# Kernel tuning notes

Measured on AMD Instinct MI355X. Metric: run time of the kernel, lower is better.

Reference implementation:

```python
import jax, jax.numpy as jnp
import numpy as np

H = 2048
EPS = 1e-5

def _layernorm(x, g, b):
    mu = jnp.mean(x, axis=-1, keepdims=True)
    var = jnp.mean(jnp.square(x - mu), axis=-1, keepdims=True)
    return (x - mu) * jax.lax.rsqrt(var + EPS) * g + b

def setup_inputs() -> dict:
    key = jax.random.key(0)
    ks = jax.random.split(key, 12)
    s = 1.0 / np.sqrt(H)
    inp = {
        "x": jax.random.normal(ks[0], (2, 2048, H), dtype=jnp.float32),
        "ln1_g": jnp.ones((H,), jnp.float32),
        "ln1_b": jnp.zeros((H,), jnp.float32),
        "ln2_g": jnp.ones((H,), jnp.float32),
        "ln2_b": jnp.zeros((H,), jnp.float32),
        "qkv_w": jax.random.uniform(ks[1], (H, 3 * H), jnp.float32, -s, s),
        "qkv_b": jax.random.uniform(ks[2], (3 * H,), jnp.float32, -s, s),
        "out_w": jax.random.uniform(ks[3], (H, H), jnp.float32, -s, s),
        "out_b": jax.random.uniform(ks[4], (H,), jnp.float32, -s, s),
        "mlp_w1": jax.random.uniform(ks[5], (H, 4 * H), jnp.float32, -s, s),
        "mlp_b1": jax.random.uniform(ks[6], (4 * H,), jnp.float32, -s, s),
        "mlp_w2": jax.random.uniform(ks[7], (4 * H, H), jnp.float32, -1.0 / np.sqrt(4 * H), 1.0 / np.sqrt(4 * H)),
        "mlp_b2": jax.random.uniform(ks[8], (H,), jnp.float32, -1.0 / np.sqrt(4 * H), 1.0 / np.sqrt(4 * H)),
    }
    return inp

def reference(x, ln1_g, ln1_b, ln2_g, ln2_b, qkv_w, qkv_b, out_w, out_b, mlp_w1, mlp_b1, mlp_w2, mlp_b2):
    residual = x
    h = _layernorm(x, ln1_g, ln1_b)
    qkv = h @ qkv_w + qkv_b                      # [B,S,3H]
    q, k, v = jnp.split(qkv, 3, axis=-1)         # each [B,S,H] (single-head attention)
    scores = jnp.einsum('bsh,bth->bst', q, k) / jnp.sqrt(jnp.float32(H))
    attn = jax.nn.softmax(scores, axis=-1)
    attn_out = jnp.einsum('bst,bth->bsh', attn, v)
    attn_out = attn_out @ out_w + out_b
    x = residual + attn_out                      # dropout is identity in eval
    residual = x
    h = _layernorm(x, ln2_g, ln2_b)
    h = jax.nn.gelu(h @ mlp_w1 + mlp_b1, approximate=False)
    h = h @ mlp_w2 + mlp_b2
    return residual + h
```

## Files before the change

### kernel.cpp

```cpp
#include <hip/hip_runtime.h>
#include <hip/hip_bf16.h>
#include <math.h>

typedef __bf16 bf16_t;
typedef __bf16 bf16x8 __attribute__((ext_vector_type(8)));
typedef __bf16 bf16x4 __attribute__((ext_vector_type(4)));
typedef float  f32x4  __attribute__((ext_vector_type(4)));

enum { EPI_BF16_BIAS = 0, EPI_F32_SCALE = 1, EPI_BF16 = 2, EPI_F32_BIAS_RES = 3, EPI_BF16_BIAS_GELU = 4 };

__device__ __forceinline__ float gelu_exact(float v) {
  return 0.5f * v * (1.0f + erff(v * 0.7071067811865476f));
}

__device__ __forceinline__ void gld_lds16(const bf16_t* g, bf16_t* l) {
  __builtin_amdgcn_global_load_lds(
      (const __attribute__((address_space(1))) uint32_t*)(uintptr_t)g,
      (__attribute__((address_space(3))) uint32_t*)(uintptr_t)l, 16, 0, 0);
}

#define SB()    __builtin_amdgcn_s_barrier()
#define LGKM0() do { asm volatile("s_waitcnt lgkmcnt(0)" ::: "memory"); __builtin_amdgcn_sched_barrier(0); } while(0)
#define VMW(N)  asm volatile("s_waitcnt vmcnt(" #N ")" ::: "memory")

#define MFMA16(BASE) do { \
  __builtin_amdgcn_s_setprio(1); \
  _Pragma("unroll") for (int ii = 0; ii < 4; ++ii) \
  _Pragma("unroll") for (int jj = 0; jj < 4; ++jj) \
    acc[(BASE)+ii][jj] = __builtin_amdgcn_mfma_f32_16x16x32_bf16(aF[ii], bF[jj], acc[(BASE)+ii][jj], 0, 0, 0); \
  __builtin_amdgcn_s_setprio(0); } while(0)

template<int EPI>
__global__ __launch_bounds__(512, 2) void tb_gemm8(
    const bf16_t* __restrict__ A, int lda, long long strideA,
    const bf16_t* __restrict__ B, int ldb, long long strideB,
    const float* __restrict__ bias,
    const float* __restrict__ resid,
    void* __restrict__ Cp, int ldc, long long strideC,
    int K, float scale)
{
  __shared__ __align__(16) bf16_t sm[65536];

  const int tid = threadIdx.x;
  const int lane = tid & 63;
  const int wid = tid >> 6;
  const int wm = wid >> 2;
  const int wn = wid & 3;
  const int lr = lane & 15;
  const int lg = lane >> 4;
  const int z = blockIdx.z;
  const int m0 = blockIdx.y * 256;
  const int n0 = blockIdx.x * 256;

  const bf16_t* Ag = A + (size_t)z * strideA + (size_t)m0 * lda;
  const bf16_t* Bg = B + (size_t)z * strideB + (size_t)n0 * ldb;

  const int sr0 = (wid << 5) + (lane >> 2);
  const int sl  = ((((lane & 3) - (lane >> 3)) & 3) << 3);
  const int sdst = (wid << 10) + lane * 8;

  const int rdo = lr * 32 + (((lg + (lr >> 1)) & 3) << 3);
  const int wmo = wm * 512;
  const int wno = wn * 512;

  f32x4 acc[8][4];
#pragma unroll
  for (int i = 0; i < 8; ++i)
#pragma unroll
    for (int j = 0; j < 4; ++j) acc[i][j] = (f32x4){0.f, 0.f, 0.f, 0.f};

  auto stageA = [&](bf16_t* region, int kc) {
    gld_lds16(Ag + (size_t)sr0 * lda + kc + sl, region + sdst);
    gld_lds16(Ag + (size_t)(sr0 + 16) * lda + kc + sl, region + sdst + 512);
  };
  auto stageB = [&](bf16_t* region, int kc) {
    gld_lds16(Bg + (size_t)sr0 * ldb + kc + sl, region + sdst);
    gld_lds16(Bg + (size_t)(sr0 + 16) * ldb + kc + sl, region + sdst + 512);
  };

  const int NT = K >> 6;
  stageA(sm + 0, 0);
  stageB(sm + 16384, 0);
  stageA(sm + 8192, 32);
  stageB(sm + 24576, 32);
  stageB(sm + 32768 + 16384, 64);
  stageA(sm + 32768 + 0, 64);
  stageB(sm + 32768 + 24576, 96);
  VMW(6);
  SB();

  bf16x8 aF[4], bF[4];

  auto tile = [&](int t, bf16_t* cur, bf16_t* oth) {
#pragma unroll
    for (int jj = 0; jj < 4; ++jj) bF[jj] = *(const bf16x8*)(cur + 16384 + jj * 2048 + wno + rdo);
#pragma unroll
    for (int ii = 0; ii < 4; ++ii) aF[ii] = *(const bf16x8*)(cur + 0 + ii * 1024 + wmo + rdo);
    if (t + 1 < NT) stageA(oth + 8192, ((t + 1) << 6) + 32);
    SB(); LGKM0();
    MFMA16(0);
    SB();
#pragma unroll
    for (int ii = 0; ii < 4; ++ii) aF[ii] = *(const bf16x8*)(cur + 4096 + ii * 1024 + wmo + rdo);
    if (t + 2 < NT) stageB(cur + 16384, (t + 2) << 6);
    SB(); LGKM0();
    MFMA16(4);
    SB();
#pragma unroll
    for (int jj = 0; jj < 4; ++jj) bF[jj] = *(const bf16x8*)(cur + 24576 + jj * 2048 + wno + rdo);
#pragma unroll
    for (int ii = 0; ii < 4; ++ii) aF[ii] = *(const bf16x8*)(cur + 8192 + ii * 1024 + wmo + rdo);
    if (t + 2 < NT) stageA(cur + 0, (t + 2) << 6);
    SB(); LGKM0();
    MFMA16(0);
    SB();
#pragma unroll
    for (int ii = 0; ii < 4; ++ii) aF[ii] = *(const bf16x8*)(cur + 12288 + ii * 1024 + wmo + rdo);
    if (t + 2 < NT) { stageB(cur + 24576, ((t + 2) << 6) + 32); VMW(6); }
    else if (t + 1 < NT) { VMW(0); }
    SB(); LGKM0();
    MFMA16(4);
    SB();
  };

  for (int t = 0; t < NT; t += 2) {
    tile(t, sm, sm + 32768);
    tile(t + 1, sm + 32768, sm);
  }

#pragma unroll
  for (int i = 0; i < 8; ++i) {
    const int mr = ((i >> 2) << 7) + ((i & 3) << 5) + (wm << 4);
#pragma unroll
    for (int j = 0; j < 4; ++j) {
      const int nc = j * 64 + (wn << 4);
#pragma unroll
      for (int r = 0; r < 4; ++r) {
        int row = m0 + mr + lg * 4 + r;
        int col = n0 + nc + lr;
        float v = acc[i][j][r] * scale;
        if constexpr (EPI == EPI_BF16_BIAS || EPI == EPI_F32_BIAS_RES || EPI == EPI_BF16_BIAS_GELU)
          v += bias[col];
        if constexpr (EPI == EPI_BF16_BIAS_GELU)
          v = gelu_exact(v);
        if constexpr (EPI == EPI_F32_BIAS_RES)
          v += resid[(size_t)row * ldc + col];
        if constexpr (EPI == EPI_BF16_BIAS || EPI == EPI_BF16 || EPI == EPI_BF16_BIAS_GELU) {
          ((bf16_t*)Cp)[(size_t)z * strideC + (size_t)row * ldc + col] = (bf16_t)v;
        } else {
          ((float*)Cp)[(size_t)z * strideC + (size_t)row * ldc + col] = v;
        }
      }
    }
  }
}

__global__ __launch_bounds__(256) void tb_combine(
    const float* __restrict__ x2, const float* __restrict__ p0,
    const float* __restrict__ p1, const float* __restrict__ bias,
    float* __restrict__ out)
{
  size_t o = ((size_t)blockIdx.x * 256 + threadIdx.x) * 4;
  float4 a = *(const float4*)(x2 + o);
  float4 b = *(const float4*)(p0 + o);
  float4 c = *(const float4*)(p1 + o);
  float4 bb = *(const float4*)(bias + (o & 2047));
  float4 r;
  r.x = a.x + b.x + c.x + bb.x;
  r.y = a.y + b.y + c.y + bb.y;
  r.z = a.z + b.z + c.z + bb.z;
  r.w = a.w + b.w + c.w + bb.w;
  *(float4*)(out + o) = r;
}

__global__ __launch_bounds__(256) void tb_transpose_cast(
    const float* __restrict__ in, bf16_t* __restrict__ outT, int R, int C)
{
  __shared__ float tile[32][33];
  int c0 = blockIdx.x * 32;
  int r0 = blockIdx.y * 32;
  int t = threadIdx.x;
  int r = t >> 3;
  int c4 = (t & 7) * 4;
  float4 d = *(const float4*)(in + (size_t)(r0 + r) * C + c0 + c4);
  tile[r][c4 + 0] = d.x; tile[r][c4 + 1] = d.y; tile[r][c4 + 2] = d.z; tile[r][c4 + 3] = d.w;
  __syncthreads();
  int c = t >> 3;
  int r4 = (t & 7) * 4;
  bf16x4 o;
  o[0] = (bf16_t)tile[r4 + 0][c];
  o[1] = (bf16_t)tile[r4 + 1][c];
  o[2] = (bf16_t)tile[r4 + 2][c];
  o[3] = (bf16_t)tile[r4 + 3][c];
  *(bf16x4*)(outT + (size_t)(c0 + c) * R + r0 + r4) = o;
}

__global__ __launch_bounds__(256) void tb_transpose_bf16(
    const bf16_t* __restrict__ in, int ldin, long long sIn,
    bf16_t* __restrict__ out, int ldout, long long sOut)
{
  __shared__ bf16_t tile[32][40];
  int z = blockIdx.z;
  const bf16_t* src = in + (size_t)z * sIn;
  bf16_t* dst = out + (size_t)z * sOut;
  int c0 = blockIdx.x * 32;
  int r0 = blockIdx.y * 32;
  int t = threadIdx.x;
  int r = t >> 3;
  int c4 = (t & 7) * 4;
  bf16x4 d = *(const bf16x4*)(src + (size_t)(r0 + r) * ldin + c0 + c4);
  *(bf16x4*)&tile[r][c4] = d;
  __syncthreads();
  int c = t >> 3;
  int r4 = (t & 7) * 4;
  bf16x4 o;
  o[0] = tile[r4 + 0][c];
  o[1] = tile[r4 + 1][c];
  o[2] = tile[r4 + 2][c];
  o[3] = tile[r4 + 3][c];
  *(bf16x4*)(dst + (size_t)(c0 + c) * ldout + r0 + r4) = o;
}

__global__ __launch_bounds__(256) void tb_layernorm(
    const float* __restrict__ x, const float* __restrict__ g, const float* __restrict__ b,
    bf16_t* __restrict__ h)
{
  __shared__ float sa[4], sb[4];
  int row = blockIdx.x;
  int t = threadIdx.x;
  const float* xr = x + (size_t)row * 2048;
  float4 v0 = *(const float4*)(xr + t * 8);
  float4 v1 = *(const float4*)(xr + t * 8 + 4);
  float a[8] = {v0.x, v0.y, v0.z, v0.w, v1.x, v1.y, v1.z, v1.w};
  float s = 0.f, q = 0.f;
#pragma unroll
  for (int j = 0; j < 8; ++j) { s += a[j]; q += a[j] * a[j]; }
#pragma unroll
  for (int o = 32; o; o >>= 1) { s += __shfl_down(s, o); q += __shfl_down(q, o); }
  int w = t >> 6, l = t & 63;
  if (l == 0) { sa[w] = s; sb[w] = q; }
  __syncthreads();
  if (t == 0) {
    sa[0] = sa[0] + sa[1] + sa[2] + sa[3];
    sb[0] = sb[0] + sb[1] + sb[2] + sb[3];
  }
  __syncthreads();
  float mu = sa[0] * (1.0f / 2048.0f);
  float var = sb[0] * (1.0f / 2048.0f) - mu * mu;
  float rs = rsqrtf(var + 1e-5f);
  float4 g0 = *(const float4*)(g + t * 8);
  float4 g1 = *(const float4*)(g + t * 8 + 4);
  float4 b0 = *(const float4*)(b + t * 8);
  float4 b1 = *(const float4*)(b + t * 8 + 4);
  float gv[8] = {g0.x, g0.y, g0.z, g0.w, g1.x, g1.y, g1.z, g1.w};
  float bv[8] = {b0.x, b0.y, b0.z, b0.w, b1.x, b1.y, b1.z, b1.w};
  bf16x8 o8;
#pragma unroll
  for (int j = 0; j < 8; ++j) o8[j] = (bf16_t)((a[j] - mu) * rs * gv[j] + bv[j]);
  *(bf16x8*)(h + (size_t)row * 2048 + t * 8) = o8;
}

__global__ __launch_bounds__(256) void tb_softmax(
    const float* __restrict__ S, bf16_t* __restrict__ P)
{
  __shared__ float sa[4];
  int row = blockIdx.x;
  int t = threadIdx.x;
  const float* sr = S + (size_t)row * 2048;
  float4 a0 = *(const float4*)(sr + t * 8);
  float4 a1 = *(const float4*)(sr + t * 8 + 4);
  float v[8] = {a0.x, a0.y, a0.z, a0.w, a1.x, a1.y, a1.z, a1.w};
  float m = v[0];
#pragma unroll
  for (int j = 1; j < 8; ++j) m = fmaxf(m, v[j]);
#pragma unroll
  for (int o = 32; o; o >>= 1) m = fmaxf(m, __shfl_down(m, o));
  int w = t >> 6, l = t & 63;
  if (l == 0) sa[w] = m;
  __syncthreads();
  if (t == 0) sa[0] = fmaxf(fmaxf(sa[0], sa[1]), fmaxf(sa[2], sa[3]));
  __syncthreads();
  m = sa[0];
  __syncthreads();
  float s = 0.f;
#pragma unroll
  for (int j = 0; j < 8; ++j) { v[j] = expf(v[j] - m); s += v[j]; }
#pragma unroll
  for (int o = 32; o; o >>= 1) s += __shfl_down(s, o);
  if (l == 0) sa[w] = s;
  __syncthreads();
  if (t == 0) sa[0] = sa[0] + sa[1] + sa[2] + sa[3];
  __syncthreads();
  float inv = 1.0f / sa[0];
  bf16x8 o8;
#pragma unroll
  for (int j = 0; j < 8; ++j) o8[j] = (bf16_t)(v[j] * inv);
  *(bf16x8*)(P + (size_t)row * 2048 + t * 8) = o8;
}

extern "C" void kernel_launch(void* const* d_in, const int* in_sizes, int n_in,
                              void* d_out, int out_size, void* d_ws, size_t ws_size,
                              hipStream_t stream) {
  const float* x     = (const float*)d_in[0];
  const float* ln1_g = (const float*)d_in[1];
  const float* ln1_b = (const float*)d_in[2];
  const float* ln2_g = (const float*)d_in[3];
  const float* ln2_b = (const float*)d_in[4];
  const float* qkv_w = (const float*)d_in[5];
  const float* qkv_b = (const float*)d_in[6];
  const float* out_w = (const float*)d_in[7];
  const float* out_b = (const float*)d_in[8];
  const float* w1    = (const float*)d_in[9];
  const float* b1    = (const float*)d_in[10];
  const float* w2    = (const float*)d_in[11];
  const float* b2    = (const float*)d_in[12];
  float* out = (float*)d_out;
  char* ws = (char*)d_ws;

  bf16_t* qkv_wT = (bf16_t*)(ws + 0);
  bf16_t* out_wT = (bf16_t*)(ws + 25165824);
  bf16_t* w1T    = (bf16_t*)(ws + 33554432);
  bf16_t* w2T    = (bf16_t*)(ws + 67108864);
  bf16_t* h_bf   = (bf16_t*)(ws + 100663296);
  bf16_t* qkv_bf = (bf16_t*)(ws + 117440512);
  float*  scores = (float*)(ws + 167772160);
  bf16_t* attn_bf= (bf16_t*)(ws + 201326592);
  bf16_t* ao_bf  = (bf16_t*)(ws + 218103808);
  float*  x2     = (float*)(ws + 234881024);
  bf16_t* mid_bf = (bf16_t*)(ws + 117440512);
  bf16_t* Vt     = (bf16_t*)(ws + 234881024);
  float*  part0  = (float*)(ws + 0);
  float*  part1  = (float*)(ws + 201326592);

  const float inv_sqrt_h = 0.022097086912079608f;

  tb_transpose_cast<<<dim3(6144 / 32, 2048 / 32), 256, 0, stream>>>(qkv_w, qkv_wT, 2048, 6144);
  tb_transpose_cast<<<dim3(2048 / 32, 2048 / 32), 256, 0, stream>>>(out_w, out_wT, 2048, 2048);
  tb_transpose_cast<<<dim3(8192 / 32, 2048 / 32), 256, 0, stream>>>(w1, w1T, 2048, 8192);
  tb_transpose_cast<<<dim3(2048 / 32, 8192 / 32), 256, 0, stream>>>(w2, w2T, 8192, 2048);

  tb_layernorm<<<4096, 256, 0, stream>>>(x, ln1_g, ln1_b, h_bf);

  tb_gemm8<EPI_BF16_BIAS><<<dim3(24, 16, 1), 512, 0, stream>>>(
      h_bf, 2048, 0, qkv_wT, 2048, 0, qkv_b, nullptr, qkv_bf, 6144, 0, 2048, 1.0f);

  tb_transpose_bf16<<<dim3(64, 64, 2), 256, 0, stream>>>(
      qkv_bf + 4096, 6144, 2048LL * 6144, Vt, 2048, 2048LL * 2048);

  tb_gemm8<EPI_F32_SCALE><<<dim3(8, 8, 2), 512, 0, stream>>>(
      qkv_bf, 6144, 2048LL * 6144, qkv_bf + 2048, 6144, 2048LL * 6144,
      nullptr, nullptr, scores, 2048, 2048LL * 2048, 2048, inv_sqrt_h);

  tb_softmax<<<4096, 256, 0, stream>>>(scores, attn_bf);

  tb_gemm8<EPI_BF16><<<dim3(8, 8, 2), 512, 0, stream>>>(
      attn_bf, 2048, 2048LL * 2048, Vt, 2048, 2048LL * 2048,
      nullptr, nullptr, ao_bf, 2048, 2048LL * 2048, 2048, 1.0f);

  tb_gemm8<EPI_F32_BIAS_RES><<<dim3(8, 16, 1), 512, 0, stream>>>(
      ao_bf, 2048, 0, out_wT, 2048, 0, out_b, x, x2, 2048, 0, 2048, 1.0f);

  tb_layernorm<<<4096, 256, 0, stream>>>(x2, ln2_g, ln2_b, h_bf);

  tb_gemm8<EPI_BF16_BIAS_GELU><<<dim3(32, 16, 1), 512, 0, stream>>>(
      h_bf, 2048, 0, w1T, 2048, 0, b1, nullptr, mid_bf, 8192, 0, 2048, 1.0f);

  tb_gemm8<EPI_F32_SCALE><<<dim3(8, 16, 2), 512, 0, stream>>>(
      mid_bf, 8192, 4096, w2T, 8192, 4096,
      nullptr, nullptr, part0, 2048, 50331648LL, 4096, 1.0f);

  tb_combine<<<8192, 256, 0, stream>>>(x2, part0, part1, b2, out);
}
```

Measured before the change: 793.3 us.

## Use XOR-swizzled 64-wide LDS tiles and remap workgroups across XCDs

Changes the LDS layout from two 32-wide k-halves per tile to full 64-wide rows with an XOR swizzle on 16-byte chunks. The global-to-LDS staging and fragment reads are rewritten to match, and the prefetch schedule is reshuffled so the next B tile and half of A are issued in the last phase. Workgroup IDs are also remapped round-robin across eight chiplets to improve L2 locality. This reduces LDS bank conflicts and changes the memory access pattern, but staging now bunches more loads into one phase, which could hurt overlap.

```diff
diff --git a/kernel.cpp b/kernel.cpp
--- a/kernel.cpp
+++ b/kernel.cpp
@@ -29,6 +29,9 @@
   _Pragma("unroll") for (int jj = 0; jj < 4; ++jj) \
     acc[(BASE)+ii][jj] = __builtin_amdgcn_mfma_f32_16x16x32_bf16(aF[ii], bF[jj], acc[(BASE)+ii][jj], 0, 0, 0); \
   __builtin_amdgcn_s_setprio(0); } while(0)
+
+#define RDA(buf, rowbase, ks) (*(const bf16x8*)((buf) + ((rowbase) + lr) * 64 + (((((ks) << 2) | lg) ^ l7) << 3)))
+#define RDB(buf, rowbase, ks) (*(const bf16x8*)((buf) + 16384 + ((rowbase) + lr) * 64 + (((((ks) << 2) | lg) ^ l7) << 3)))
 
 template<int EPI>
 __global__ __launch_bounds__(512, 2) void tb_gemm8(
@@ -48,20 +51,23 @@
   const int wn = wid & 3;
   const int lr = lane & 15;
   const int lg = lane >> 4;
-  const int z = blockIdx.z;
-  const int m0 = blockIdx.y * 256;
-  const int n0 = blockIdx.x * 256;
+  const int l7 = lr & 7;
+
+  const int gx = gridDim.x, gy = gridDim.y;
+  const int nwg = gx * gy * gridDim.z;
+  int lin = blockIdx.x + gx * (blockIdx.y + gy * blockIdx.z);
+  lin = (lin & 7) * (nwg >> 3) + (lin >> 3);
+  const int bx = lin % gx;
+  const int by = (lin / gx) % gy;
+  const int z  = lin / (gx * gy);
+  const int m0 = by * 256, n0 = bx * 256;
 
   const bf16_t* Ag = A + (size_t)z * strideA + (size_t)m0 * lda;
   const bf16_t* Bg = B + (size_t)z * strideB + (size_t)n0 * ldb;
 
-  const int sr0 = (wid << 5) + (lane >> 2);
-  const int sl  = ((((lane & 3) - (lane >> 3)) & 3) << 3);
-  const int sdst = (wid << 10) + lane * 8;
-
-  const int rdo = lr * 32 + (((lg + (lr >> 1)) & 3) << 3);
-  const int wmo = wm * 512;
-  const int wno = wn * 512;
+  const int l8 = lane >> 3;
+  const int ssw = (((lane & 7) ^ l8) << 3);
+  const int c0 = wid << 1;
 
   f32x4 acc[8][4];
 #pragma unroll
@@ -69,63 +75,72 @@
 #pragma unroll
     for (int j = 0; j < 4; ++j) acc[i][j] = (f32x4){0.f, 0.f, 0.f, 0.f};
 
-  auto stageA = [&](bf16_t* region, int kc) {
-    gld_lds16(Ag + (size_t)sr0 * lda + kc + sl, region + sdst);
-    gld_lds16(Ag + (size_t)(sr0 + 16) * lda + kc + sl, region + sdst + 512);
+  auto stA = [&](bf16_t* buf, int h, int kt) {
+#pragma unroll
+    for (int q = 0; q < 2; ++q) {
+      int rb = (h << 7) + ((c0 + q) << 3);
+      gld_lds16(Ag + (size_t)(rb + l8) * lda + kt + ssw, buf + rb * 64 + lane * 8);
+    }
   };
-  auto stageB = [&](bf16_t* region, int kc) {
-    gld_lds16(Bg + (size_t)sr0 * ldb + kc + sl, region + sdst);
-    gld_lds16(Bg + (size_t)(sr0 + 16) * ldb + kc + sl, region + sdst + 512);
+  auto stB = [&](bf16_t* buf, int h, int kt) {
+#pragma unroll
+    for (int q = 0; q < 2; ++q) {
+      int rb = (h << 7) + ((c0 + q) << 3);
+      gld_lds16(Bg + (size_t)(rb + l8) * ldb + kt + ssw, buf + 16384 + rb * 64 + lane * 8);
+    }
   };
 
   const int NT = K >> 6;
-  stageA(sm + 0, 0);
-  stageB(sm + 16384, 0);
-  stageA(sm + 8192, 32);
-  stageB(sm + 24576, 32);
-  stageB(sm + 32768 + 16384, 64);
-  stageA(sm + 32768 + 0, 64);
-  stageB(sm + 32768 + 24576, 96);
+  bf16_t* buf0 = sm;
+  bf16_t* buf1 = sm + 32768;
+
+  stA(buf0, 0, 0); stB(buf0, 0, 0); stB(buf0, 1, 0); stA(buf0, 1, 0);
+  stB(buf1, 0, 64); stB(buf1, 1, 64); stA(buf1, 0, 64);
   VMW(6);
   SB();
 
   bf16x8 aF[4], bF[4];
 
   auto tile = [&](int t, bf16_t* cur, bf16_t* oth) {
-#pragma unroll
-    for (int jj = 0; jj < 4; ++jj) bF[jj] = *(const bf16x8*)(cur + 16384 + jj * 2048 + wno + rdo);
-#pragma unroll
-    for (int ii = 0; ii < 4; ++ii) aF[ii] = *(const bf16x8*)(cur + 0 + ii * 1024 + wmo + rdo);
-    if (t + 1 < NT) stageA(oth + 8192, ((t + 1) << 6) + 32);
+    const int ktn = (t + 2) << 6;
+#pragma unroll
+    for (int jj = 0; jj < 4; ++jj) bF[jj] = RDB(cur, jj * 64 + wn * 16, 0);
+#pragma unroll
+    for (int ii = 0; ii < 4; ++ii) aF[ii] = RDA(cur, ii * 32 + wm * 16, 0);
+    if (t + 1 < NT) stA(oth, 1, (t + 1) << 6);
     SB(); LGKM0();
     MFMA16(0);
     SB();
 #pragma unroll
-    for (int ii = 0; ii < 4; ++ii) aF[ii] = *(const bf16x8*)(cur + 4096 + ii * 1024 + wmo + rdo);
-    if (t + 2 < NT) stageB(cur + 16384, (t + 2) << 6);
+    for (int ii = 0; ii < 4; ++ii) aF[ii] = RDA(cur, 128 + ii * 32 + wm * 16, 0);
     SB(); LGKM0();
     MFMA16(4);
     SB();
 #pragma unroll
-    for (int jj = 0; jj < 4; ++jj) bF[jj] = *(const bf16x8*)(cur + 24576 + jj * 2048 + wno + rdo);
-#pragma unroll
-    for (int ii = 0; ii < 4; ++ii) aF[ii] = *(const bf16x8*)(cur + 8192 + ii * 1024 + wmo + rdo);
-    if (t + 2 < NT) stageA(cur + 0, (t + 2) << 6);
+    for (int jj = 0; jj < 4; ++jj) bF[jj] = RDB(cur, jj * 64 + wn * 16, 1);
+#pragma unroll
+    for (int ii = 0; ii < 4; ++ii) aF[ii] = RDA(cur, ii * 32 + wm * 16, 1);
     SB(); LGKM0();
     MFMA16(0);
     SB();
 #pragma unroll
-    for (int ii = 0; ii < 4; ++ii) aF[ii] = *(const bf16x8*)(cur + 12288 + ii * 1024 + wmo + rdo);
-    if (t + 2 < NT) { stageB(cur + 24576, ((t + 2) << 6) + 32); VMW(6); }
-    else if (t + 1 < NT) { VMW(0); }
+    for (int ii = 0; ii < 4; ++ii) aF[ii] = RDA(cur, 128 + ii * 32 + wm * 16, 1);
+    if (t + 2 < NT) {
+      stB(cur, 0, ktn);
+      stB(cur, 1, ktn);
+      stA(cur, 0, ktn);
+      VMW(6);
+    } else if (t + 1 < NT) {
+      VMW(0);
+    }
     SB(); LGKM0();
     MFMA16(4);
     SB();
   };
 
   for (int t = 0; t < NT; t += 2) {
-    tile(t, sm, sm + 32768);
-    tile(t + 1, sm + 32768, sm);
+    tile(t, buf0, buf1);
+    tile(t + 1, buf1, buf0);
   }
 
 #pragma unroll
```

Result: slower. 1.498 ms (+88.8%).
